# Kernel optimization log

Measured on AMD Instinct MI355X. Metric: run time of the kernel, lower is better.

The kernel has to match this reference:

```python
import jax, jax.numpy as jnp
import numpy as np

N_EMBED = 2048
N_HEAD = 16
N_GROUP = 4
D_HEAD = N_EMBED // N_HEAD  # 128
GROUP_SIZE = N_HEAD // N_GROUP  # 4
SLIDING_WINDOW = 512
ATTENTION_SINK = 4
POS = 0
ROPE_BASE = 10000.0


def _rope(x, pos):
    # x: (B, T, H, d) -> rotate-half RoPE applied along last dim
    B, T, H, d = x.shape
    half = d // 2
    inv_freq = 1.0 / (ROPE_BASE ** (jnp.arange(half, dtype=jnp.float32) * 2.0 / d))
    t = jnp.arange(T, dtype=jnp.float32) + pos
    ang = t[:, None] * inv_freq[None, :]           # (T, half)
    cos = jnp.cos(ang)[None, :, None, :].astype(x.dtype)
    sin = jnp.sin(ang)[None, :, None, :].astype(x.dtype)
    x1, x2 = x[..., :half], x[..., half:]
    return jnp.concatenate([x1 * cos - x2 * sin, x1 * sin + x2 * cos], axis=-1)


def _sliding_mask(q_len, kv_len):
    i = jnp.arange(q_len)[:, None]
    j = jnp.arange(kv_len)[None, :]
    causal = i >= j
    sink = j < ATTENTION_SINK
    local = j >= i - SLIDING_WINDOW
    return causal & (local | sink)  # (q_len, kv_len) bool


def setup_inputs() -> dict:
    key = jax.random.key(0)
    ks = jax.random.split(key, 9)
    s_in = 1.0 / np.sqrt(N_EMBED)
    x = jax.random.normal(ks[0], (2, 2048, N_EMBED), dtype=jnp.float32)
    # Linear weights stored as (in, out): y = x @ W + b
    Wq = jax.random.uniform(ks[1], (N_EMBED, N_HEAD * D_HEAD), jnp.float32, -s_in, s_in)
    bq = jax.random.uniform(ks[2], (N_HEAD * D_HEAD,), jnp.float32, -s_in, s_in)
    Wk = jax.random.uniform(ks[3], (N_EMBED, N_GROUP * D_HEAD), jnp.float32, -s_in, s_in)
    bk = jax.random.uniform(ks[4], (N_GROUP * D_HEAD,), jnp.float32, -s_in, s_in)
    Wv = jax.random.uniform(ks[5], (N_EMBED, N_GROUP * D_HEAD), jnp.float32, -s_in, s_in)
    bv = jax.random.uniform(ks[6], (N_GROUP * D_HEAD,), jnp.float32, -s_in, s_in)
    Wo = jax.random.uniform(ks[7], (N_EMBED, N_EMBED), jnp.float32, -s_in, s_in)
    bo = jax.random.uniform(ks[8], (N_EMBED,), jnp.float32, -s_in, s_in)
    return {"x": x, "Wq": Wq, "bq": bq, "Wk": Wk, "bk": bk,
            "Wv": Wv, "bv": bv, "Wo": Wo, "bo": bo}


def reference(x, Wq, bq, Wk, bk, Wv, bv, Wo, bo):
    B, T, C = x.shape
    scale = D_HEAD ** -0.5
    Q = (x @ Wq + bq).reshape(B, T, N_HEAD, D_HEAD)
    K = (x @ Wk + bk).reshape(B, T, N_GROUP, D_HEAD)
    V = (x @ Wv + bv).reshape(B, T, N_GROUP, D_HEAD)
    Q = _rope(Q, POS)
    K = _rope(K, POS)
    # (B, G, group, T, d) -- native GQA broadcast instead of repeat_interleave
    Q = Q.transpose(0, 2, 1, 3).reshape(B, N_GROUP, GROUP_SIZE, T, D_HEAD)
    K = K.transpose(0, 2, 1, 3)  # (B, G, T, d)
    V = V.transpose(0, 2, 1, 3)
    scores = jnp.einsum('bghtd,bgsd->bghts', Q, K) * scale  # (B,G,h,T,S)
    mask = _sliding_mask(T, T)[None, None, None, :, :]
    neg = jnp.finfo(scores.dtype).min
    scores = jnp.where(mask, scores, neg)
    W = jax.nn.softmax(scores, axis=-1)
    out = jnp.einsum('bghts,bgsd->bghtd', W, V)  # (B,G,h,T,d)
    out = out.reshape(B, N_HEAD, T, D_HEAD).transpose(0, 2, 1, 3).reshape(B, T, C)
    return out @ Wo + bo
```

## Files before the change

### kernel.cpp

```cpp
#include <hip/hip_runtime.h>
#include <hip/hip_bf16.h>
#include <cstdint>
#include <cstddef>


typedef short s16;
typedef short short8 __attribute__((ext_vector_type(8)));
typedef short s16x4  __attribute__((ext_vector_type(4)));
typedef float f32x4  __attribute__((ext_vector_type(4)));

#define MFMA16(a, b, c) __builtin_amdgcn_mfma_f32_16x16x32_bf16((a), (b), (c), 0, 0, 0)

__device__ __forceinline__ float bf2f(s16 u) {
    union { float f; uint32_t i; } v;
    v.i = ((uint32_t)(uint16_t)u) << 16;
    return v.f;
}
__device__ __forceinline__ s16 f2bf(float f) {
    union { float f; uint32_t i; } v;
    v.f = f;
    uint32_t r = v.i + 0x7FFFu + ((v.i >> 16) & 1u);
    return (s16)(r >> 16);
}

__device__ __forceinline__ uint32_t cvtpk_bf16(float lo, float hi) {
    uint32_t r;
    asm("v_cvt_pk_bf16_f32 %0, %1, %2" : "=v"(r) : "v"(lo), "v"(hi));
    return r;
}

__device__ __forceinline__ void gload16(const s16* g, s16* l) {
    __builtin_amdgcn_global_load_lds(
        (const __attribute__((address_space(1))) void*)g,
        (__attribute__((address_space(3))) void*)l, 16, 0, 0);
}

__global__ __launch_bounds__(256)
void cast_bf16(const float* __restrict__ in, s16* __restrict__ out)
{
    size_t i = ((size_t)blockIdx.x * 256 + threadIdx.x) * 8;
    f32x4 f0 = *(const f32x4*)(in + i);
    f32x4 f1 = *(const f32x4*)(in + i + 4);
    short8 h;
    h[0]=f2bf(f0[0]); h[1]=f2bf(f0[1]); h[2]=f2bf(f0[2]); h[3]=f2bf(f0[3]);
    h[4]=f2bf(f1[0]); h[5]=f2bf(f1[1]); h[6]=f2bf(f1[2]); h[7]=f2bf(f1[3]);
    *(short8*)(out + i) = h;
}

__global__ __launch_bounds__(256)
void castT3(const float* __restrict__ Wq, const float* __restrict__ Wk,
            const float* __restrict__ Wv, s16* __restrict__ out)
{
    int z = blockIdx.z;
    const float* in; s16* dst; int N;
    if (z == 0)      { in = Wq; dst = out;                        N = 2048; }
    else if (z == 1) { in = Wk; dst = out + (size_t)2048 * 2048;  N = 512; }
    else             { in = Wv; dst = out + (size_t)2560 * 2048;  N = 512; }
    int n0 = blockIdx.x * 32, k0 = blockIdx.y * 32;
    if (n0 >= N) return;

    __shared__ float t[32][33];
    int tx = threadIdx.x & 31, ty = threadIdx.x >> 5;
    for (int i = 0; i < 32; i += 8)
        t[ty + i][tx] = in[(size_t)(k0 + ty + i) * N + n0 + tx];
    __syncthreads();
    for (int i = 0; i < 32; i += 8)
        dst[(size_t)(n0 + ty + i) * 2048 + k0 + tx] = f2bf(t[tx][ty + i]);
}

__global__ __launch_bounds__(256)
void castT(const float* __restrict__ in, s16* __restrict__ out)
{
    __shared__ float t[32][33];
    int n0 = blockIdx.x * 32, k0 = blockIdx.y * 32;
    int tx = threadIdx.x & 31, ty = threadIdx.x >> 5;
    for (int i = 0; i < 32; i += 8)
        t[ty + i][tx] = in[(size_t)(k0 + ty + i) * 2048 + n0 + tx];
    __syncthreads();
    for (int i = 0; i < 32; i += 8)
        out[(size_t)(n0 + ty + i) * 2048 + k0 + tx] = f2bf(t[tx][ty + i]);
}

template <int MODE>
__global__ __launch_bounds__(256, 3)
void gemm_bk64(const s16* __restrict__ A, const s16* __restrict__ Bt,
               const float* __restrict__ b0, const float* __restrict__ b1,
               const float* __restrict__ b2,
               void* __restrict__ o0, void* __restrict__ o1, void* __restrict__ o2,
               int M, int N, int K)
{
    __shared__ s16 As[128 * 64];
    __shared__ s16 Bs[128 * 64];

    const int tid  = threadIdx.x;
    const int lane = tid & 63, wv = tid >> 6;
    const int m0 = blockIdx.x * 128, n0 = blockIdx.y * 128;
    const int wm = (wv >> 1) * 64, wn = (wv & 1) * 64;
    const int fr = lane & 15, fq = lane >> 4;
    const int NT = K >> 6;

    const int srow = tid >> 3;
    const int scol = ((tid & 7) ^ (srow & 7)) << 3;
    const s16* gA[4];
    const s16* gB[4];
    #pragma unroll
    for (int s = 0; s < 4; s++) {
        gA[s] = A  + (size_t)(m0 + s * 32 + srow) * K + scol;
        gB[s] = Bt + (size_t)(n0 + s * 32 + srow) * K + scol;
    }

    const int kc0 = (fq ^ (fr & 7)) << 4;
    const int kc1 = kc0 ^ 64;
    const char* aRow = (const char*)As + (wm + fr) * 128;
    const char* bRow = (const char*)Bs + (wn + fr) * 128;

    f32x4 acc[4][4] = {};

    for (int t = 0; t < NT; t++) {
        __syncthreads();
        #pragma unroll
        for (int s = 0; s < 4; s++)
            gload16(gA[s] + t * 64, As + s * 2048 + wv * 512);
        #pragma unroll
        for (int s = 0; s < 4; s++)
            gload16(gB[s] + t * 64, Bs + s * 2048 + wv * 512);
        __syncthreads();

        short8 af[4][2], bfr[4][2];
        #pragma unroll
        for (int mi = 0; mi < 4; mi++) {
            af[mi][0] = *(const short8*)(aRow + mi * 2048 + kc0);
            af[mi][1] = *(const short8*)(aRow + mi * 2048 + kc1);
        }
        #pragma unroll
        for (int ni = 0; ni < 4; ni++) {
            bfr[ni][0] = *(const short8*)(bRow + ni * 2048 + kc0);
            bfr[ni][1] = *(const short8*)(bRow + ni * 2048 + kc1);
        }

        __builtin_amdgcn_s_setprio(1);
        #pragma unroll
        for (int mi = 0; mi < 4; mi++)
            #pragma unroll
            for (int ni = 0; ni < 4; ni++) {
                acc[mi][ni] = MFMA16(af[mi][0], bfr[ni][0], acc[mi][ni]);
                acc[mi][ni] = MFMA16(af[mi][1], bfr[ni][1], acc[mi][ni]);
            }
        __builtin_amdgcn_s_setprio(0);
    }

    #pragma unroll
    for (int mi = 0; mi < 4; mi++)
        #pragma unroll
        for (int ni = 0; ni < 4; ni++)
            #pragma unroll
            for (int r = 0; r < 4; r++) {
                int m = m0 + wm + mi * 16 + fq * 4 + r;
                int n = n0 + wn + ni * 16 + fr;
                float v = acc[mi][ni][r];
                if (MODE == 0) {
                    if (n < 2048)
                        ((s16*)o0)[(size_t)m * 2048 + n] = f2bf(v + b0[n]);
                    else if (n < 2560)
                        ((s16*)o1)[(size_t)m * 512 + (n - 2048)] = f2bf(v + b1[n - 2048]);
                    else
                        ((s16*)o2)[(size_t)(n - 2560) * 4096 + m] = f2bf(v + b2[n - 2560]);
                } else {
                    ((float*)o0)[(size_t)m * N + n] = v + b0[n];
                }
            }
}

__global__ __launch_bounds__(256)
void rope2_kernel(s16* __restrict__ Qb, s16* __restrict__ Kb)
{
    int bx = blockIdx.x;
    s16* buf; int nheads; int idx;
    if (bx < 16384) { buf = Qb; nheads = 16; idx = bx * 256 + threadIdx.x; }
    else            { buf = Kb; nheads = 4;  idx = (bx - 16384) * 256 + threadIdx.x; }

    int i   = idx & 63;
    int hi  = idx >> 6;
    int h   = hi % nheads;
    int row = hi / nheads;
    int t   = row & 2047;

    float inv_freq = __powf(10000.0f, -(float)i * (1.0f / 64.0f));
    float ang = (float)t * inv_freq;
    float c = cosf(ang);
    float s = sinf(ang);

    size_t base = (size_t)row * ((size_t)nheads * 128) + (size_t)h * 128 + i;
    float x1 = bf2f(buf[base]);
    float x2 = bf2f(buf[base + 64]);
    buf[base]      = f2bf(x1 * c - x2 * s);
    buf[base + 64] = f2bf(x1 * s + x2 * c);
}

__global__ __launch_bounds__(256)
void attn_kernel(const s16* __restrict__ Q, const s16* __restrict__ Kb,
                 const s16* __restrict__ Vt, s16* __restrict__ At)
{
    __shared__ s16 Ks[2][32][136];
    __shared__ s16 Vs[2][128][40];
    __shared__ s16 Ps[4][16][40];

    const int b = blockIdx.z;
    const int h = blockIdx.y, g = h >> 2;
    const int t0 = (31 - blockIdx.x) * 64;
    const int tid = threadIdx.x, lane = tid & 63, wv = tid >> 6;
    const int fr = lane & 15, fq = lane >> 4;
    const int tw = t0 + wv * 16;
    s16* O = At + (size_t)b * 4194304;

    const float SCL2 = 0.12751743f;
    const float NEG  = -1e9f;
    const float THR2 = 11.541560f;

    int kr[2], kc[2], vd[2], vc[2];
    const s16 *gK[2], *gV[2];
    #pragma unroll
    for (int it = 0; it < 2; it++) {
        int idx = it * 2048 + tid * 8;
        kr[it] = idx >> 7;  kc[it] = idx & 127;
        vd[it] = idx >> 5;  vc[it] = idx & 31;
        gK[it] = Kb + (size_t)(b * 2048 + kr[it]) * 512 + g * 128 + kc[it];
        gV[it] = Vt + (size_t)(g * 128 + vd[it]) * 4096 + b * 2048 + vc[it];
    }

    short8 qf[4];
    {
        const s16* qrow = Q + (size_t)(b * 2048 + tw + fr) * 2048 + h * 128 + fq * 8;
        qf[0] = *(const short8*)(qrow);
        qf[1] = *(const short8*)(qrow + 32);
        qf[2] = *(const short8*)(qrow + 64);
        qf[3] = *(const short8*)(qrow + 96);
    }

    f32x4 Oacc[8] = {};
    float m2 = NEG, l_s = 0.0f;
    const int tq = tw + fr;

    int lo = t0 - 512; if (lo < 0) lo = 0;
    const int c0   = lo >> 5;
    const int cend = (t0 + 63) >> 5;
    const int nch  = cend - c0 + 1 + (c0 > 0 ? 1 : 0);

    #define CHUNKBASE(ic) ((((c0) > 0) ? ((ic) == 0 ? 0 : c0 + (ic) - 1) : (ic)) * 32)

    short8 kpre[2], vpre[2];
    {
        int kb = CHUNKBASE(0);
        #pragma unroll
        for (int it = 0; it < 2; it++) {
            kpre[it] = *(const short8*)(gK[it] + (size_t)kb * 512);
            vpre[it] = *(const short8*)(gV[it] + kb);
        }
        #pragma unroll
        for (int it = 0; it < 2; it++) {
            *(short8*)&Ks[0][kr[it]][kc[it]] = kpre[it];
            *(short8*)&Vs[0][vd[it]][vc[it]] = vpre[it];
        }
    }
    __syncthreads();

    for (int ic = 0; ic < nch; ic++) {
        const int cur = ic & 1;
        const int kbase = CHUNKBASE(ic);
        const bool pre = (ic + 1 < nch);
        if (pre) {
            int kb = CHUNKBASE(ic + 1);
            #pragma unroll
            for (int it = 0; it < 2; it++) {
                kpre[it] = *(const short8*)(gK[it] + (size_t)kb * 512);
                vpre[it] = *(const short8*)(gV[it] + kb);
            }
        }

        f32x4 sc[2] = {{0.f,0.f,0.f,0.f},{0.f,0.f,0.f,0.f}};
        __builtin_amdgcn_s_setprio(1);
        #pragma unroll
        for (int kn = 0; kn < 2; kn++)
            #pragma unroll
            for (int dc = 0; dc < 4; dc++) {
                short8 kf = *(const short8*)&Ks[cur][kn * 16 + fr][dc * 32 + fq * 8];
                sc[kn] = MFMA16(kf, qf[dc], sc[kn]);
            }
        __builtin_amdgcn_s_setprio(0);

        const bool fast = (kbase + 31 <= tw) && (kbase >= tw + 15 - 512);

        float sv[8], cm;
        if (fast) {
            #pragma unroll
            for (int i = 0; i < 4; i++) { sv[i] = sc[0][i]; sv[4 + i] = sc[1][i]; }
            float a0 = fmaxf(sv[0], sv[1]), a1 = fmaxf(sv[2], sv[3]);
            float a2 = fmaxf(sv[4], sv[5]), a3 = fmaxf(sv[6], sv[7]);
            cm = fmaxf(fmaxf(a0, a1), fmaxf(a2, a3)) * SCL2;
        } else {
            #pragma unroll
            for (int kn = 0; kn < 2; kn++)
                #pragma unroll
                for (int r = 0; r < 4; r++) {
                    int j = kbase + kn * 16 + fq * 4 + r;
                    bool ok = (j <= tq) && ((j >= tq - 512) || (j < 4));
                    sv[kn * 4 + r] = ok ? sc[kn][r] * SCL2 : NEG;
                }
            cm = fmaxf(sv[0], sv[1]);
            #pragma unroll
            for (int i = 2; i < 8; i++) cm = fmaxf(cm, sv[i]);
        }
        cm = fmaxf(cm, __shfl_xor(cm, 16));
        cm = fmaxf(cm, __shfl_xor(cm, 32));

        if (__any(cm > m2 + THR2)) {
            float nm    = fmaxf(m2, cm);
            float alpha = exp2f(m2 - nm);
            m2  = nm;
            l_s *= alpha;
            #pragma unroll
            for (int r = 0; r < 4; r++) {
                float ar = __shfl(alpha, (lane & 48) + fq * 4 + r);
                #pragma unroll
                for (int n0 = 0; n0 < 8; n0++) Oacc[n0][r] *= ar;
            }
        }

        float p[8], ps = 0.0f;
        if (fast) {
            const float nm2 = -m2;
            #pragma unroll
            for (int i = 0; i < 8; i++) { p[i] = exp2f(fmaf(sv[i], SCL2, nm2)); ps += p[i]; }
        } else {
            #pragma unroll
            for (int i = 0; i < 8; i++) { p[i] = exp2f(sv[i] - m2); ps += p[i]; }
        }
        ps += __shfl_xor(ps, 16);
        ps += __shfl_xor(ps, 32);
        l_s += ps;

        union { s16x4 v; uint32_t u[2]; } w0, w1;
        w0.u[0] = cvtpk_bf16(p[0], p[1]);
        w0.u[1] = cvtpk_bf16(p[2], p[3]);
        w1.u[0] = cvtpk_bf16(p[4], p[5]);
        w1.u[1] = cvtpk_bf16(p[6], p[7]);
        *(s16x4*)&Ps[wv][fr][fq * 4]      = w0.v;
        *(s16x4*)&Ps[wv][fr][16 + fq * 4] = w1.v;
        __threadfence_block();
        short8 pf = *(const short8*)&Ps[wv][fr][fq * 8];

        __builtin_amdgcn_s_setprio(1);
        #pragma unroll
        for (int n0 = 0; n0 < 8; n0++) {
            short8 vf = *(const short8*)&Vs[cur][n0 * 16 + fr][fq * 8];
            Oacc[n0] = MFMA16(pf, vf, Oacc[n0]);
        }
        __builtin_amdgcn_s_setprio(0);

        if (pre) {
            #pragma unroll
            for (int it = 0; it < 2; it++) {
                *(short8*)&Ks[cur ^ 1][kr[it]][kc[it]] = kpre[it];
                *(short8*)&Vs[cur ^ 1][vd[it]][vc[it]] = vpre[it];
            }
            __syncthreads();
        }
    }

    float linv[4];
    #pragma unroll
    for (int r = 0; r < 4; r++)
        linv[r] = 1.0f / __shfl(l_s, (lane & 48) + fq * 4 + r);
    #pragma unroll
    for (int n0 = 0; n0 < 8; n0++)
        #pragma unroll
        for (int r = 0; r < 4; r++) {
            int t = tw + fq * 4 + r;
            O[(size_t)t * 2048 + h * 128 + n0 * 16 + fr] =
                f2bf(Oacc[n0][r] * linv[r]);
        }
}

extern "C" void kernel_launch(void* const* d_in, const int* in_sizes, int n_in,
                              void* d_out, int out_size, void* d_ws, size_t ws_size,
                              hipStream_t stream)
{
    const float* x  = (const float*)d_in[0];
    const float* Wq = (const float*)d_in[1];
    const float* bq = (const float*)d_in[2];
    const float* Wk = (const float*)d_in[3];
    const float* bk = (const float*)d_in[4];
    const float* Wv = (const float*)d_in[5];
    const float* bv = (const float*)d_in[6];
    const float* Wo = (const float*)d_in[7];
    const float* bo = (const float*)d_in[8];
    float* out = (float*)d_out;

    if (ws_size < 33554432) return;

    char* ws = (char*)d_ws;
    s16* xb    = (s16*)(ws + 0);
    s16* At    = (s16*)(ws + 0);
    s16* Wqkvt = (s16*)(ws + 16777216);
    s16* Wot   = (s16*)(ws + 16777216);
    s16* Qb    = (s16*)d_out;
    s16* Kb    = (s16*)((char*)d_out + 16777216);
    s16* Vt    = (s16*)((char*)d_out + 20971520);

    cast_bf16<<<4096, 256, 0, stream>>>(x, xb);

    castT3<<<dim3(64, 64, 3), 256, 0, stream>>>(Wq, Wk, Wv, Wqkvt);

    gemm_bk64<0><<<dim3(32, 24), 256, 0, stream>>>(xb, Wqkvt, bq, bk, bv,
                                                   Qb, Kb, Vt, 4096, 3072, 2048);

    rope2_kernel<<<20480, 256, 0, stream>>>(Qb, Kb);

    castT<<<dim3(64, 64), 256, 0, stream>>>(Wo, Wot);

    attn_kernel<<<dim3(32, 16, 2), 256, 0, stream>>>(Qb, Kb, Vt, At);

    gemm_bk64<2><<<dim3(32, 16), 256, 0, stream>>>(At, Wot, bo, nullptr, nullptr,
                                                   out, nullptr, nullptr,
                                                   4096, 2048, 2048);
}
```

Measured before the change: 305.3 us.

## Fuse RoPE into QKV GEMM epilogue, merge prep kernels, swizzle attention LDS

Applies RoPE inside the QKV GEMM epilogue. The right-half columns are exchanged through LDS so each wave can rotate its pairs, using a precomputed cos/sin table, and the separate rope kernel is removed. The x cast, weight transposes and table build are merged into one prep launch. The attention kernel's K, V and P shared tiles move to XOR-swizzled unpadded layouts to cut bank conflicts. Together these remove a full read/write pass over Q/K and two launches, at the cost of a more complex epilogue with an extra LDS exchange and syncs.

```diff
diff --git a/kernel.cpp b/kernel.cpp
--- a/kernel.cpp
+++ b/kernel.cpp
@@ -36,26 +36,35 @@
 }
 
 __global__ __launch_bounds__(256)
-void cast_bf16(const float* __restrict__ in, s16* __restrict__ out)
-{
-    size_t i = ((size_t)blockIdx.x * 256 + threadIdx.x) * 8;
-    f32x4 f0 = *(const f32x4*)(in + i);
-    f32x4 f1 = *(const f32x4*)(in + i + 4);
-    short8 h;
-    h[0]=f2bf(f0[0]); h[1]=f2bf(f0[1]); h[2]=f2bf(f0[2]); h[3]=f2bf(f0[3]);
-    h[4]=f2bf(f1[0]); h[5]=f2bf(f1[1]); h[6]=f2bf(f1[2]); h[7]=f2bf(f1[3]);
-    *(short8*)(out + i) = h;
-}
-
-__global__ __launch_bounds__(256)
-void castT3(const float* __restrict__ Wq, const float* __restrict__ Wk,
-            const float* __restrict__ Wv, s16* __restrict__ out)
+void prep(const float* __restrict__ Wq, const float* __restrict__ Wk,
+          const float* __restrict__ Wv, const float* __restrict__ x,
+          s16* __restrict__ wout, float2* __restrict__ tab,
+          s16* __restrict__ xb)
 {
     int z = blockIdx.z;
+    if (z == 4) {
+        size_t i = ((size_t)(blockIdx.x * 64 + blockIdx.y) * 256 + threadIdx.x) * 8;
+        f32x4 f0 = *(const f32x4*)(x + i);
+        f32x4 f1 = *(const f32x4*)(x + i + 4);
+        short8 h;
+        h[0]=f2bf(f0[0]); h[1]=f2bf(f0[1]); h[2]=f2bf(f0[2]); h[3]=f2bf(f0[3]);
+        h[4]=f2bf(f1[0]); h[5]=f2bf(f1[1]); h[6]=f2bf(f1[2]); h[7]=f2bf(f1[3]);
+        *(short8*)(xb + i) = h;
+        return;
+    }
+    if (z == 3) {
+        if (blockIdx.x >= 8) return;
+        int e = (blockIdx.x * 64 + blockIdx.y) * 256 + threadIdx.x;
+        int t = e >> 6, i = e & 63;
+        float inv = __powf(10000.0f, -(float)i * (1.0f / 64.0f));
+        float ang = (float)t * inv;
+        tab[e] = make_float2(cosf(ang), sinf(ang));
+        return;
+    }
     const float* in; s16* dst; int N;
-    if (z == 0)      { in = Wq; dst = out;                        N = 2048; }
-    else if (z == 1) { in = Wk; dst = out + (size_t)2048 * 2048;  N = 512; }
-    else             { in = Wv; dst = out + (size_t)2560 * 2048;  N = 512; }
+    if (z == 0)      { in = Wq; dst = wout;                        N = 2048; }
+    else if (z == 1) { in = Wk; dst = wout + (size_t)2048 * 2048;  N = 512; }
+    else             { in = Wv; dst = wout + (size_t)2560 * 2048;  N = 512; }
     int n0 = blockIdx.x * 32, k0 = blockIdx.y * 32;
     if (n0 >= N) return;
 
@@ -85,7 +94,7 @@
 __global__ __launch_bounds__(256, 3)
 void gemm_bk64(const s16* __restrict__ A, const s16* __restrict__ Bt,
                const float* __restrict__ b0, const float* __restrict__ b1,
-               const float* __restrict__ b2,
+               const float* __restrict__ b2, const float2* __restrict__ tab,
                void* __restrict__ o0, void* __restrict__ o1, void* __restrict__ o2,
                int M, int N, int K)
 {
@@ -149,6 +158,54 @@
         __builtin_amdgcn_s_setprio(0);
     }
 
+    if (MODE == 0 && n0 < 2560) {
+        const bool qreg = (n0 < 2048);
+        float* xch = (float*)(wm ? Bs : As);
+        __syncthreads();
+        if (wn) {
+            #pragma unroll
+            for (int mi = 0; mi < 4; mi++)
+                #pragma unroll
+                for (int ni = 0; ni < 4; ni++)
+                    #pragma unroll
+                    for (int r = 0; r < 4; r++) {
+                        int n = n0 + 64 + ni * 16 + fr;
+                        float bv = qreg ? b0[n] : b1[n - 2048];
+                        xch[(mi * 16 + fq * 4 + r) * 64 + ni * 16 + fr] =
+                            acc[mi][ni][r] + bv;
+                    }
+        }
+        __syncthreads();
+        if (!wn) {
+            #pragma unroll
+            for (int mi = 0; mi < 4; mi++)
+                #pragma unroll
+                for (int ni = 0; ni < 4; ni++)
+                    #pragma unroll
+                    for (int r = 0; r < 4; r++) {
+                        int m = m0 + wm + mi * 16 + fq * 4 + r;
+                        int n = n0 + ni * 16 + fr;
+                        int i = ni * 16 + fr;
+                        float bv = qreg ? b0[n] : b1[n - 2048];
+                        float x1 = acc[mi][ni][r] + bv;
+                        float x2 = xch[(mi * 16 + fq * 4 + r) * 64 + i];
+                        float2 cs = tab[(size_t)(m & 2047) * 64 + i];
+                        float ro1 = x1 * cs.x - x2 * cs.y;
+                        float ro2 = x1 * cs.y + x2 * cs.x;
+                        if (qreg) {
+                            s16* q = (s16*)o0;
+                            q[(size_t)m * 2048 + n]      = f2bf(ro1);
+                            q[(size_t)m * 2048 + n + 64] = f2bf(ro2);
+                        } else {
+                            s16* k = (s16*)o1;
+                            k[(size_t)m * 512 + (n - 2048)]      = f2bf(ro1);
+                            k[(size_t)m * 512 + (n - 2048) + 64] = f2bf(ro2);
+                        }
+                    }
+        }
+        return;
+    }
+
     #pragma unroll
     for (int mi = 0; mi < 4; mi++)
         #pragma unroll
@@ -159,51 +216,20 @@
                 int n = n0 + wn + ni * 16 + fr;
                 float v = acc[mi][ni][r];
                 if (MODE == 0) {
-                    if (n < 2048)
-                        ((s16*)o0)[(size_t)m * 2048 + n] = f2bf(v + b0[n]);
-                    else if (n < 2560)
-                        ((s16*)o1)[(size_t)m * 512 + (n - 2048)] = f2bf(v + b1[n - 2048]);
-                    else
-                        ((s16*)o2)[(size_t)(n - 2560) * 4096 + m] = f2bf(v + b2[n - 2560]);
+                    ((s16*)o2)[(size_t)(n - 2560) * 4096 + m] = f2bf(v + b2[n - 2560]);
                 } else {
                     ((float*)o0)[(size_t)m * N + n] = v + b0[n];
                 }
             }
-}
-
-__global__ __launch_bounds__(256)
-void rope2_kernel(s16* __restrict__ Qb, s16* __restrict__ Kb)
-{
-    int bx = blockIdx.x;
-    s16* buf; int nheads; int idx;
-    if (bx < 16384) { buf = Qb; nheads = 16; idx = bx * 256 + threadIdx.x; }
-    else            { buf = Kb; nheads = 4;  idx = (bx - 16384) * 256 + threadIdx.x; }
-
-    int i   = idx & 63;
-    int hi  = idx >> 6;
-    int h   = hi % nheads;
-    int row = hi / nheads;
-    int t   = row & 2047;
-
-    float inv_freq = __powf(10000.0f, -(float)i * (1.0f / 64.0f));
-    float ang = (float)t * inv_freq;
-    float c = cosf(ang);
-    float s = sinf(ang);
-
-    size_t base = (size_t)row * ((size_t)nheads * 128) + (size_t)h * 128 + i;
-    float x1 = bf2f(buf[base]);
-    float x2 = bf2f(buf[base + 64]);
-    buf[base]      = f2bf(x1 * c - x2 * s);
-    buf[base + 64] = f2bf(x1 * s + x2 * c);
 }
 
 __global__ __launch_bounds__(256)
 void attn_kernel(const s16* __restrict__ Q, const s16* __restrict__ Kb,
                  const s16* __restrict__ Vt, s16* __restrict__ At)
 {
-    __shared__ s16 Ks[2][32][136];
-    __shared__ s16 Vs[2][128][40];
-    __shared__ s16 Ps[4][16][40];
+    __shared__ s16 Ks[2][64][64];
+    __shared__ s16 Vs[2][64][64];
+    __shared__ s16 Ps[4][8][64];
 
     const int b = blockIdx.z;
     const int h = blockIdx.y, g = h >> 2;
@@ -217,16 +243,30 @@
     const float NEG  = -1e9f;
     const float THR2 = 11.541560f;
 
-    int kr[2], kc[2], vd[2], vc[2];
+    int kwoff[2], vwoff[2];
     const s16 *gK[2], *gV[2];
     #pragma unroll
     for (int it = 0; it < 2; it++) {
-        int idx = it * 2048 + tid * 8;
-        kr[it] = idx >> 7;  kc[it] = idx & 127;
-        vd[it] = idx >> 5;  vc[it] = idx & 31;
-        gK[it] = Kb + (size_t)(b * 2048 + kr[it]) * 512 + g * 128 + kc[it];
-        gV[it] = Vt + (size_t)(g * 128 + vd[it]) * 4096 + b * 2048 + vc[it];
-    }
+        int idx  = it * 2048 + tid * 8;
+        int key  = idx >> 7, d = idx & 127;
+        int krow = key + 32 * (d >> 6);
+        kwoff[it] = krow * 128 + ((((d >> 3) & 7) ^ (key & 7)) << 4);
+        int vd   = idx >> 5, vkey = idx & 31;
+        int vrow = vd >> 1;
+        vwoff[it] = vrow * 128 +
+                    (((((vd & 1) * 4 + (vkey >> 3)) ^ (vrow & 7))) << 4);
+        gK[it] = Kb + (size_t)(b * 2048 + key) * 512 + g * 128 + d;
+        gV[it] = Vt + (size_t)(g * 128 + vd) * 4096 + b * 2048 + vkey;
+    }
+
+    const int kc0 = (fq ^ (fr & 7)) << 4;
+    const int kc1 = kc0 ^ 64;
+    const int vc0 = ((((fr & 1) * 4 + fq) ^ ((fr >> 1) & 7)) << 4);
+    const int pw0 = (fr >> 1) * 128 +
+                    ((((fr & 1) * 4 + (fq >> 1)) ^ ((fr >> 1) & 7)) << 4) +
+                    (fq & 1) * 8;
+    const int pw1 = pw0 ^ 32;
+    char* psbase = (char*)&Ps[wv][0][0];
 
     short8 qf[4];
     {
@@ -258,8 +298,8 @@
         }
         #pragma unroll
         for (int it = 0; it < 2; it++) {
-            *(short8*)&Ks[0][kr[it]][kc[it]] = kpre[it];
-            *(short8*)&Vs[0][vd[it]][vc[it]] = vpre[it];
+            *(short8*)((char*)&Ks[0][0][0] + kwoff[it]) = kpre[it];
+            *(short8*)((char*)&Vs[0][0][0] + vwoff[it]) = vpre[it];
         }
     }
     __syncthreads();
@@ -277,13 +317,15 @@
             }
         }
 
+        const char* kbl = (const char*)&Ks[cur][0][0] + fr * 128;
         f32x4 sc[2] = {{0.f,0.f,0.f,0.f},{0.f,0.f,0.f,0.f}};
         __builtin_amdgcn_s_setprio(1);
         #pragma unroll
         for (int kn = 0; kn < 2; kn++)
             #pragma unroll
             for (int dc = 0; dc < 4; dc++) {
-                short8 kf = *(const short8*)&Ks[cur][kn * 16 + fr][dc * 32 + fq * 8];
+                short8 kf = *(const short8*)(kbl + kn * 2048 + (dc >> 1) * 4096
+                                             + ((dc & 1) ? kc1 : kc0));
                 sc[kn] = MFMA16(kf, qf[dc], sc[kn]);
             }
         __builtin_amdgcn_s_setprio(0);
@@ -344,15 +386,16 @@
         w0.u[1] = cvtpk_bf16(p[2], p[3]);
         w1.u[0] = cvtpk_bf16(p[4], p[5]);
         w1.u[1] = cvtpk_bf16(p[6], p[7]);
-        *(s16x4*)&Ps[wv][fr][fq * 4]      = w0.v;
-        *(s16x4*)&Ps[wv][fr][16 + fq * 4] = w1.v;
+        *(s16x4*)(psbase + pw0) = w0.v;
+        *(s16x4*)(psbase + pw1) = w1.v;
         __threadfence_block();
-        short8 pf = *(const short8*)&Ps[wv][fr][fq * 8];
+        short8 pf = *(const short8*)(psbase + (fr >> 1) * 128 + vc0);
 
         __builtin_amdgcn_s_setprio(1);
+        const char* vbl = (const char*)&Vs[cur][0][0] + (fr >> 1) * 128 + vc0;
         #pragma unroll
         for (int n0 = 0; n0 < 8; n0++) {
-            short8 vf = *(const short8*)&Vs[cur][n0 * 16 + fr][fq * 8];
+            short8 vf = *(const short8*)(vbl + n0 * 1024);
             Oacc[n0] = MFMA16(pf, vf, Oacc[n0]);
         }
         __builtin_amdgcn_s_setprio(0);
@@ -360,8 +403,8 @@
         if (pre) {
             #pragma unroll
             for (int it = 0; it < 2; it++) {
-                *(short8*)&Ks[cur ^ 1][kr[it]][kc[it]] = kpre[it];
-                *(short8*)&Vs[cur ^ 1][vd[it]][vc[it]] = vpre[it];
+                *(short8*)((char*)&Ks[cur ^ 1][0][0] + kwoff[it]) = kpre[it];
+                *(short8*)((char*)&Vs[cur ^ 1][0][0] + vwoff[it]) = vpre[it];
             }
             __syncthreads();
         }
@@ -403,24 +446,21 @@
     s16* At    = (s16*)(ws + 0);
     s16* Wqkvt = (s16*)(ws + 16777216);
     s16* Wot   = (s16*)(ws + 16777216);
+    float2* tab = (float2*)(ws + 29360128);
     s16* Qb    = (s16*)d_out;
     s16* Kb    = (s16*)((char*)d_out + 16777216);
     s16* Vt    = (s16*)((char*)d_out + 20971520);
 
-    cast_bf16<<<4096, 256, 0, stream>>>(x, xb);
-
-    castT3<<<dim3(64, 64, 3), 256, 0, stream>>>(Wq, Wk, Wv, Wqkvt);
-
-    gemm_bk64<0><<<dim3(32, 24), 256, 0, stream>>>(xb, Wqkvt, bq, bk, bv,
+    prep<<<dim3(64, 64, 5), 256, 0, stream>>>(Wq, Wk, Wv, x, Wqkvt, tab, xb);
+
+    gemm_bk64<0><<<dim3(32, 24), 256, 0, stream>>>(xb, Wqkvt, bq, bk, bv, tab,
                                                    Qb, Kb, Vt, 4096, 3072, 2048);
 
-    rope2_kernel<<<20480, 256, 0, stream>>>(Qb, Kb);
-
     castT<<<dim3(64, 64), 256, 0, stream>>>(Wo, Wot);
 
     attn_kernel<<<dim3(32, 16, 2), 256, 0, stream>>>(Qb, Kb, Vt, At);
 
     gemm_bk64<2><<<dim3(32, 16), 256, 0, stream>>>(At, Wot, bo, nullptr, nullptr,
-                                                   out, nullptr, nullptr,
+                                                   nullptr, out, nullptr, nullptr,
                                                    4096, 2048, 2048);
 }
```

Result: faster. 290.0 us (-5.0%).
